# Optimization experiments

Measured on AMD Instinct MI355X. Metric: run time of the kernel, lower is better.

Reference implementation:

```python
import jax, jax.numpy as jnp
import numpy as np

E, B, L, H1, H2, C = 8, 4096, 512, 1024, 512, 40


def setup_inputs() -> dict:
    key = jax.random.key(0)
    ks = jax.random.split(key, 9)
    return {
        "x_s": jax.random.normal(ks[0], (B, L), jnp.float32),
        "x_p": jax.random.normal(ks[1], (B, L), jnp.float32),
        "W1": jax.random.normal(ks[2], (E, 2 * L, H1), jnp.float32) / np.sqrt(2 * L).astype(np.float32),
        "b1": jax.random.normal(ks[3], (E, H1), jnp.float32) * 0.01,
        "W2": jax.random.normal(ks[4], (E, H1, H2), jnp.float32) / np.sqrt(H1).astype(np.float32),
        "b2": jax.random.normal(ks[5], (E, H2), jnp.float32) * 0.01,
        "W3": jax.random.normal(ks[6], (E, H2, C), jnp.float32) / np.sqrt(H2).astype(np.float32),
        "b3": jax.random.normal(ks[7], (E, C), jnp.float32) * 0.01,
        "sub_module_label": jax.random.randint(ks[8], (B,), 0, E, dtype=jnp.int32),
        "sub_id": 0,
    }


def reference(x_s, x_p, W1, b1, W2, b2, W3, b3, sub_module_label, sub_id):
    # Encoders (EEGNet/SCN/DCN) abstracted as identity: x_s / x_p are latent features.
    # Cls_HEAD.forward: x = cat([x_p, x_s], dim=1); per-sample routed 3-layer ELU MLP head.
    # Dropout is identity in eval mode.
    x = jnp.concatenate([x_p, x_s], axis=1)                      # [B, 2L]
    h = jax.nn.elu(jnp.einsum('bi,eih->ebh', x, W1) + b1[:, None, :])   # [E, B, H1]
    h = jax.nn.elu(jnp.einsum('ebh,ehk->ebk', h, W2) + b2[:, None, :])  # [E, B, H2]
    out_all = jnp.einsum('ebk,ekc->ebc', h, W3) + b3[:, None, :]        # [E, B, C]
    # select each sample's routed expert output
    bidx = jnp.arange(x.shape[0])
    return out_all[sub_module_label, bidx]                       # [B, C]
```

## Files before the change

kernel.cpp:

```cpp
#include <hip/hip_runtime.h>
#include <hip/hip_bf16.h>
#include <math.h>

#define En   8
#define Bn   4096
#define Ln   512
#define K1n  1024
#define H1n  1024
#define H2n  512
#define Cn   40
#define NP3  48
#define NTR  72

typedef unsigned short u16;
typedef __attribute__((ext_vector_type(8))) short bf16x8;
typedef __attribute__((ext_vector_type(4))) float f32x4;

__device__ __forceinline__ u16 f2b(float f) {
    union { float f; unsigned int u; } v; v.f = f;
    unsigned int r = v.u + 0x7FFF + ((v.u >> 16) & 1);
    return (u16)(r >> 16);
}

__device__ __forceinline__ void g2l16(const void* g, void* l) {
    __builtin_amdgcn_global_load_lds(
        (const __attribute__((address_space(1))) unsigned int*)(unsigned long long)g,
        (__attribute__((address_space(3))) unsigned int*)(unsigned int)(unsigned long long)l,
        16, 0, 0);
}

__device__ __forceinline__ void wtrans64(
    const float* __restrict__ Wsrc, u16* __restrict__ Wdst,
    int K, int N, int k0, int n0, int tid, float* sm )
{
    #pragma unroll
    for (int s = 0; s < 4; s++) {
        int idx = tid + s * 256;
        int kk = idx >> 4, c4 = (idx & 15) * 4;
        float4 v = *(const float4*)&Wsrc[(size_t)(k0 + kk) * N + n0 + c4];
        float* row = sm + kk * 65 + c4;
        row[0] = v.x; row[1] = v.y; row[2] = v.z; row[3] = v.w;
    }
    __syncthreads();
    #pragma unroll
    for (int s = 0; s < 4; s++) {
        int idx = tid + s * 256;
        int nn = idx >> 4, kc = (idx & 15) * 4;
        ushort4 o = make_ushort4(f2b(sm[(kc + 0) * 65 + nn]), f2b(sm[(kc + 1) * 65 + nn]),
                                 f2b(sm[(kc + 2) * 65 + nn]), f2b(sm[(kc + 3) * 65 + nn]));
        *(ushort4*)&Wdst[(size_t)(n0 + nn) * K + k0 + kc] = o;
    }
}

#define P1_TOT (1 + 256 + 2048)

__global__ __launch_bounds__(256) void prep1_kernel(
    const float* __restrict__ xs, const float* __restrict__ xp,
    const float* __restrict__ W1, const int* __restrict__ label,
    int* __restrict__ meta, int* __restrict__ perm,
    u16* __restrict__ Xb, u16* __restrict__ W1t)
{
    __shared__ __align__(16) float sm[64 * 65];
    const int bid = blockIdx.x;
    const int tid = threadIdx.x;

    if (bid == 0) {
        int* cnt = (int*)sm;
        int* off = cnt + En;
        if (tid < En) cnt[tid] = 0;
        __syncthreads();
        for (int b = tid; b < Bn; b += 256) atomicAdd(&cnt[label[b]], 1);
        __syncthreads();
        if (tid == 0) {
            int run = 0;
            for (int e = 0; e < En; e++) { off[e] = run; run += cnt[e]; }
            off[En] = run;
        }
        __syncthreads();
        if (tid < En) cnt[tid] = off[tid];
        __syncthreads();
        for (int b = tid; b < Bn; b += 256) {
            int e = label[b];
            perm[atomicAdd(&cnt[e], 1)] = b;
        }
        if (tid <= En) meta[tid] = off[tid];
    } else if (bid < 257) {
        int r0 = (bid - 1) * 16;
        #pragma unroll 4
        for (int s = 0; s < 16; s++) {
            int r = r0 + s;
            int k = tid * 4;
            const float* src = (k < Ln) ? (xp + (size_t)r * Ln + k)
                                        : (xs + (size_t)r * Ln + (k - Ln));
            float4 v = *(const float4*)src;
            *(ushort4*)&Xb[(size_t)r * K1n + k] =
                make_ushort4(f2b(v.x), f2b(v.y), f2b(v.z), f2b(v.w));
        }
    } else {
        int b = bid - 257;
        int e = b >> 8, rem = b & 255;
        int k0 = (rem >> 4) * 64, n0 = (rem & 15) * 64;
        wtrans64(W1 + (size_t)e * K1n * H1n, W1t + (size_t)e * H1n * K1n,
                 K1n, H1n, k0, n0, tid, sm);
    }
}

template <int K, int N, bool GATHER, bool FUSE3, bool PREP2>
__global__ __launch_bounds__(256) void mfma_gemm(
    const u16* __restrict__ A, const u16* __restrict__ Wt,
    const float* __restrict__ bias, const int* __restrict__ meta,
    const int* __restrict__ perm, u16* __restrict__ outb,
    const u16* __restrict__ Wt3, float* __restrict__ outf,
    const float* __restrict__ W2f, const float* __restrict__ W3f,
    const float* __restrict__ b3v, const int* __restrict__ labelv,
    u16* __restrict__ W2t_o, u16* __restrict__ W3t_o)
{
    constexpr int TM = 64, BK = 64;
    constexpr int T = K / BK;
    constexpr int NTC = N / 64;
    __shared__ __align__(16) u16 SM[16384];

    const int tid = threadIdx.x;
    const int bx = blockIdx.x;

    if (PREP2 && bx >= NTR * NTC) {
        int jb = bx - NTR * NTC;
        if (jb < 1024) {
            int e = jb >> 7, rem = jb & 127;
            int k0 = (rem >> 3) * 64, n0 = (rem & 7) * 64;
            wtrans64(W2f + (size_t)e * H1n * H2n, W2t_o + (size_t)e * H2n * H1n,
                     H1n, H2n, k0, n0, tid, (float*)SM);
        } else if (jb < 1024 + 128) {
            int b = jb - 1024;
            int e = b >> 4, k0 = (b & 15) * 32;
            const float* src = W3f + (size_t)e * H2n * Cn;
            u16* dst = W3t_o + (size_t)e * NP3 * H2n;
            float* t = (float*)SM;
            #pragma unroll
            for (int s = 0; s < 5; s++) {
                int idx = tid + s * 256;
                int kk = idx / Cn, nn = idx - kk * Cn;
                if (kk < 32) t[kk * 41 + nn] = src[(size_t)(k0 + kk) * Cn + nn];
            }
            __syncthreads();
            #pragma unroll
            for (int s = 0; s < 6; s++) {
                int idx = tid + s * 256;
                int nn = idx >> 5, kk = idx & 31;
                float v = (nn < Cn) ? t[kk * 41 + nn] : 0.f;
                dst[(size_t)nn * H2n + k0 + kk] = f2b(v);
            }
        } else {
            int b = jb - (1024 + 128);
            int r0 = b * 64;
            #pragma unroll
            for (int s = 0; s < 10; s++) {
                int idx = tid + s * 256;
                int r = r0 + idx / Cn;
                int c = idx - (idx / Cn) * Cn;
                outf[(size_t)r * Cn + c] = b3v[labelv[r] * Cn + c];
            }
        }
        return;
    }

    const int rt = bx % NTR;
    const int col0 = (bx / NTR) * 64;

    int expert = -1, row0 = 0, rowmax = 0, acc_t = 0;
    int prev = meta[0];
    #pragma unroll
    for (int e = 0; e < En; e++) {
        int nxt = meta[e + 1];
        int c = nxt - prev;
        int t = (c + TM - 1) / TM;
        if (expert < 0 && rt < acc_t + t) {
            expert = e; row0 = prev + (rt - acc_t) * TM; rowmax = nxt - 1;
        }
        acc_t += t; prev = nxt;
    }
    if (expert < 0) return;

    const u16* Wexp = Wt + (size_t)expert * N * K;

    const int lane = tid & 63;
    const int wid = tid >> 6;
    const int wm = (wid & 1) * 32;
    const int wn = (wid >> 1) * 32;
    const int l15 = lane & 15;
    const int lq = lane >> 4;

    const u16* aptr[2]; const u16* bptr[2];
    int aoff[2], boff[2];
    #pragma unroll
    for (int s = 0; s < 2; s++) {
        int idx = tid + s * 256;
        int rl = idx >> 3, c = idx & 7;
        int kq = c ^ (rl & 7);
        int rg = row0 + rl; if (rg > rowmax) rg = rowmax;
        if (GATHER) rg = perm[rg];
        aptr[s] = A + (size_t)rg * K + kq * 8;
        bptr[s] = Wexp + (size_t)(col0 + rl) * K + kq * 8;
        aoff[s] = idx * 8;
        boff[s] = 4096 + idx * 8;
    }
    const int csw = l15 & 7;

    f32x4 acc[2][2];
    #pragma unroll
    for (int i = 0; i < 2; i++)
        #pragma unroll
        for (int j = 0; j < 2; j++) acc[i][j] = (f32x4){0.f, 0.f, 0.f, 0.f};

    #pragma unroll
    for (int s = 0; s < 2; s++) {
        g2l16(aptr[s], &SM[aoff[s]]);
        g2l16(bptr[s], &SM[boff[s]]);
    }

    for (int t = 0; t < T; t++) {
        __syncthreads();
        const u16* As = &SM[(t & 1) * 8192];
        const u16* Bs = As + 4096;
        if (t + 1 < T) {
            int base = ((t + 1) & 1) * 8192;
            int ko = (t + 1) * BK;
            #pragma unroll
            for (int s = 0; s < 2; s++) {
                g2l16(aptr[s] + ko, &SM[base + aoff[s]]);
                g2l16(bptr[s] + ko, &SM[base + boff[s]]);
            }
        }
        #pragma unroll
        for (int h = 0; h < 2; h++) {
            const int ksw = ((h * 4 + lq) ^ csw) << 3;
            bf16x8 af[2], bf[2];
            #pragma unroll
            for (int i = 0; i < 2; i++)
                af[i] = *(const bf16x8*)&As[(wm + i * 16 + l15) * BK + ksw];
            #pragma unroll
            for (int j = 0; j < 2; j++)
                bf[j] = *(const bf16x8*)&Bs[(wn + j * 16 + l15) * BK + ksw];
            #pragma unroll
            for (int i = 0; i < 2; i++)
                #pragma unroll
                for (int j = 0; j < 2; j++)
                    acc[i][j] = __builtin_amdgcn_mfma_f32_16x16x32_bf16(
                        af[i], bf[j], acc[i][j], 0, 0, 0);
        }
    }

    if (!FUSE3) {
        #pragma unroll
        for (int i = 0; i < 2; i++) {
            #pragma unroll
            for (int j = 0; j < 2; j++) {
                int col = col0 + wn + j * 16 + l15;
                float bv = bias[expert * N + col];
                #pragma unroll
                for (int r = 0; r < 4; r++) {
                    int grow = row0 + wm + i * 16 + lq * 4 + r;
                    if (grow <= rowmax) {
                        float v = acc[i][j][r] + bv;
                        v = (v > 0.f) ? v : (expf(v) - 1.f);
                        outb[(size_t)grow * N + col] = f2b(v);
                    }
                }
            }
        }
    } else {
        __syncthreads();
        u16* H = &SM[0];
        #pragma unroll
        for (int i = 0; i < 2; i++) {
            #pragma unroll
            for (int j = 0; j < 2; j++) {
                int col = wn + j * 16 + l15;
                float bv = bias[expert * N + col0 + col];
                #pragma unroll
                for (int r = 0; r < 4; r++) {
                    float v = acc[i][j][r] + bv;
                    v = (v > 0.f) ? v : (expf(v) - 1.f);
                    H[(wm + i * 16 + lq * 4 + r) * 72 + col] = f2b(v);
                }
            }
        }
        __syncthreads();
        const int rh = wid * 16;
        f32x4 a3[3];
        #pragma unroll
        for (int j = 0; j < 3; j++) a3[j] = (f32x4){0.f, 0.f, 0.f, 0.f};
        #pragma unroll
        for (int ki = 0; ki < 2; ki++) {
            bf16x8 ha = *(const bf16x8*)&H[(rh + l15) * 72 + ki * 32 + lq * 8];
            #pragma unroll
            for (int j = 0; j < 3; j++) {
                bf16x8 wb = *(const bf16x8*)
                    &Wt3[((size_t)expert * NP3 + j * 16 + l15) * H2n + col0 + ki * 32 + lq * 8];
                a3[j] = __builtin_amdgcn_mfma_f32_16x16x32_bf16(ha, wb, a3[j], 0, 0, 0);
            }
        }
        #pragma unroll
        for (int j = 0; j < 3; j++) {
            int col = j * 16 + l15;
            if (col < Cn) {
                #pragma unroll
                for (int r = 0; r < 4; r++) {
                    int grow = row0 + rh + lq * 4 + r;
                    if (grow <= rowmax)
                        atomicAdd(&outf[(size_t)perm[grow] * Cn + col], a3[j][r]);
                }
            }
        }
    }
}

extern "C" void kernel_launch(void* const* d_in, const int* in_sizes, int n_in,
                              void* d_out, int out_size, void* d_ws, size_t ws_size,
                              hipStream_t stream)
{
    const float* xs = (const float*)d_in[0];
    const float* xp = (const float*)d_in[1];
    const float* W1 = (const float*)d_in[2];
    const float* b1 = (const float*)d_in[3];
    const float* W2 = (const float*)d_in[4];
    const float* b2 = (const float*)d_in[5];
    const float* W3 = (const float*)d_in[6];
    const float* b3 = (const float*)d_in[7];
    const int* label = (const int*)d_in[8];
    float* out = (float*)d_out;

    char* ws = (char*)d_ws;
    int* meta = (int*)ws;
    int* perm = (int*)(ws + 64);
    u16* Xb  = (u16*)(ws + (64 << 10));
    u16* W1t = (u16*)(ws + (64 << 10) + (8  << 20));
    u16* W2t = (u16*)(ws + (64 << 10) + (24 << 20));
    u16* h1b = (u16*)(ws + (64 << 10) + (32 << 20));
    u16* W3t = (u16*)(ws + (64 << 10) + (40 << 20));

    prep1_kernel<<<P1_TOT, 256, 0, stream>>>(
        xs, xp, W1, label, meta, perm, Xb, W1t);

    mfma_gemm<K1n, H1n, true, false, true><<<72 * 16 + 1216, 256, 0, stream>>>(
        Xb, W1t, b1, meta, perm, h1b, nullptr, out,
        W2, W3, b3, label, W2t, W3t);

    mfma_gemm<H1n, H2n, false, true, false><<<72 * 8, 256, 0, stream>>>(
        h1b, W2t, b2, meta, perm, nullptr, W3t, out,
        nullptr, nullptr, nullptr, nullptr, nullptr, nullptr);
}
```

Baseline: 168.5 us.

## Template GEMM tile sizes and switch to larger tiles with BK=32

Makes the routed MFMA GEMM tile dimensions template parameters and uses 128x128 tiles for layer 1 and 128x64 for layer 2, with the K step halved to 32 and a matching new LDS swizzle. The fused layer-3 epilogue is generalized to cover multiple 16-row groups per wave. Larger tiles raise operand reuse per block and cut redundant global/LDS traffic. The cost is fewer blocks (320 per GEMM), more padding waste at expert boundaries, and twice as many barrier iterations along K.

New measurement: 173.1 us. 2.8% more time.

```diff
diff --git a/kernel.cpp b/kernel.cpp
--- a/kernel.cpp
+++ b/kernel.cpp
@@ -10,7 +10,6 @@
 #define H2n  512
 #define Cn   40
 #define NP3  48
-#define NTR  72
 
 typedef unsigned short u16;
 typedef __attribute__((ext_vector_type(8))) short bf16x8;
@@ -105,7 +104,7 @@
     }
 }
 
-template <int K, int N, bool GATHER, bool FUSE3, bool PREP2>
+template <int K, int N, int TM, int TN, bool GATHER, bool FUSE3, bool PREP2>
 __global__ __launch_bounds__(256) void mfma_gemm(
     const u16* __restrict__ A, const u16* __restrict__ Wt,
     const float* __restrict__ bias, const int* __restrict__ meta,
@@ -115,16 +114,23 @@
     const float* __restrict__ b3v, const int* __restrict__ labelv,
     u16* __restrict__ W2t_o, u16* __restrict__ W3t_o)
 {
-    constexpr int TM = 64, BK = 64;
-    constexpr int T = K / BK;
-    constexpr int NTC = N / 64;
-    __shared__ __align__(16) u16 SM[16384];
+    constexpr int BK    = 32;
+    constexpr int T     = K / BK;
+    constexpr int NTC   = N / TN;
+    constexpr int NTRk  = Bn / TM + En;
+    constexpr int ASLOT = TM * 4;
+    constexpr int BSLOT = TN * 4;
+    constexpr int STAGE = ASLOT + BSLOT;
+    constexpr int HSTR  = TN + 8;
+    constexpr int SMST  = 2 * STAGE * 8;
+    constexpr int SMU16 = (FUSE3 && (TM * HSTR) > SMST) ? (TM * HSTR) : SMST;
+    __shared__ __align__(16) u16 SM[SMU16];
 
     const int tid = threadIdx.x;
     const int bx = blockIdx.x;
 
-    if (PREP2 && bx >= NTR * NTC) {
-        int jb = bx - NTR * NTC;
+    if (PREP2 && bx >= NTRk * NTC) {
+        int jb = bx - NTRk * NTC;
         if (jb < 1024) {
             int e = jb >> 7, rem = jb & 127;
             int k0 = (rem >> 3) * 64, n0 = (rem & 7) * 64;
@@ -164,8 +170,8 @@
         return;
     }
 
-    const int rt = bx % NTR;
-    const int col0 = (bx / NTR) * 64;
+    const int rt = bx % NTRk;
+    const int col0 = (bx / NTRk) * TN;
 
     int expert = -1, row0 = 0, rowmax = 0, acc_t = 0;
     int prev = meta[0];
@@ -185,76 +191,81 @@
 
     const int lane = tid & 63;
     const int wid = tid >> 6;
-    const int wm = (wid & 1) * 32;
-    const int wn = (wid >> 1) * 32;
+    const int wm = (wid & 1) * (TM / 2);
+    const int wn = (wid >> 1) * (TN / 2);
     const int l15 = lane & 15;
     const int lq = lane >> 4;
 
-    const u16* aptr[2]; const u16* bptr[2];
-    int aoff[2], boff[2];
-    #pragma unroll
-    for (int s = 0; s < 2; s++) {
+    constexpr int ALOAD = ASLOT / 256;
+    constexpr int BLOAD = BSLOT / 256;
+    const u16* aptr[ALOAD]; int aoff[ALOAD];
+    const u16* bptr[BLOAD]; int boff[BLOAD];
+    #pragma unroll
+    for (int s = 0; s < ALOAD; s++) {
         int idx = tid + s * 256;
-        int rl = idx >> 3, c = idx & 7;
-        int kq = c ^ (rl & 7);
+        int rl = idx >> 2, c = idx & 3;
+        int kq = c ^ ((rl >> 1) & 3);
         int rg = row0 + rl; if (rg > rowmax) rg = rowmax;
         if (GATHER) rg = perm[rg];
         aptr[s] = A + (size_t)rg * K + kq * 8;
+        aoff[s] = idx * 8;
+    }
+    #pragma unroll
+    for (int s = 0; s < BLOAD; s++) {
+        int idx = tid + s * 256;
+        int rl = idx >> 2, c = idx & 3;
+        int kq = c ^ ((rl >> 1) & 3);
         bptr[s] = Wexp + (size_t)(col0 + rl) * K + kq * 8;
-        aoff[s] = idx * 8;
-        boff[s] = 4096 + idx * 8;
-    }
-    const int csw = l15 & 7;
-
-    f32x4 acc[2][2];
-    #pragma unroll
-    for (int i = 0; i < 2; i++)
-        #pragma unroll
-        for (int j = 0; j < 2; j++) acc[i][j] = (f32x4){0.f, 0.f, 0.f, 0.f};
-
-    #pragma unroll
-    for (int s = 0; s < 2; s++) {
-        g2l16(aptr[s], &SM[aoff[s]]);
-        g2l16(bptr[s], &SM[boff[s]]);
-    }
+        boff[s] = ASLOT * 8 + idx * 8;
+    }
+
+    constexpr int MI = TM / 32;
+    constexpr int NJ = TN / 32;
+    f32x4 acc[MI][NJ];
+    #pragma unroll
+    for (int i = 0; i < MI; i++)
+        #pragma unroll
+        for (int j = 0; j < NJ; j++) acc[i][j] = (f32x4){0.f, 0.f, 0.f, 0.f};
+
+    #pragma unroll
+    for (int s = 0; s < ALOAD; s++) g2l16(aptr[s], &SM[aoff[s]]);
+    #pragma unroll
+    for (int s = 0; s < BLOAD; s++) g2l16(bptr[s], &SM[boff[s]]);
+
+    const int cp = (lq ^ ((l15 >> 1) & 3)) * 8;
 
     for (int t = 0; t < T; t++) {
         __syncthreads();
-        const u16* As = &SM[(t & 1) * 8192];
-        const u16* Bs = As + 4096;
+        const u16* As = &SM[(t & 1) * (STAGE * 8)];
+        const u16* Bs = As + ASLOT * 8;
         if (t + 1 < T) {
-            int base = ((t + 1) & 1) * 8192;
+            int base = ((t + 1) & 1) * (STAGE * 8);
             int ko = (t + 1) * BK;
             #pragma unroll
-            for (int s = 0; s < 2; s++) {
-                g2l16(aptr[s] + ko, &SM[base + aoff[s]]);
-                g2l16(bptr[s] + ko, &SM[base + boff[s]]);
-            }
-        }
-        #pragma unroll
-        for (int h = 0; h < 2; h++) {
-            const int ksw = ((h * 4 + lq) ^ csw) << 3;
-            bf16x8 af[2], bf[2];
-            #pragma unroll
-            for (int i = 0; i < 2; i++)
-                af[i] = *(const bf16x8*)&As[(wm + i * 16 + l15) * BK + ksw];
-            #pragma unroll
-            for (int j = 0; j < 2; j++)
-                bf[j] = *(const bf16x8*)&Bs[(wn + j * 16 + l15) * BK + ksw];
-            #pragma unroll
-            for (int i = 0; i < 2; i++)
-                #pragma unroll
-                for (int j = 0; j < 2; j++)
-                    acc[i][j] = __builtin_amdgcn_mfma_f32_16x16x32_bf16(
-                        af[i], bf[j], acc[i][j], 0, 0, 0);
-        }
+            for (int s = 0; s < ALOAD; s++) g2l16(aptr[s] + ko, &SM[base + aoff[s]]);
+            #pragma unroll
+            for (int s = 0; s < BLOAD; s++) g2l16(bptr[s] + ko, &SM[base + boff[s]]);
+        }
+        bf16x8 af[MI], bf[NJ];
+        #pragma unroll
+        for (int i = 0; i < MI; i++)
+            af[i] = *(const bf16x8*)&As[(wm + i * 16 + l15) * BK + cp];
+        #pragma unroll
+        for (int j = 0; j < NJ; j++)
+            bf[j] = *(const bf16x8*)&Bs[(wn + j * 16 + l15) * BK + cp];
+        #pragma unroll
+        for (int i = 0; i < MI; i++)
+            #pragma unroll
+            for (int j = 0; j < NJ; j++)
+                acc[i][j] = __builtin_amdgcn_mfma_f32_16x16x32_bf16(
+                    af[i], bf[j], acc[i][j], 0, 0, 0);
     }
 
     if (!FUSE3) {
         #pragma unroll
-        for (int i = 0; i < 2; i++) {
-            #pragma unroll
-            for (int j = 0; j < 2; j++) {
+        for (int i = 0; i < MI; i++) {
+            #pragma unroll
+            for (int j = 0; j < NJ; j++) {
                 int col = col0 + wn + j * 16 + l15;
                 float bv = bias[expert * N + col];
                 #pragma unroll
@@ -272,32 +283,42 @@
         __syncthreads();
         u16* H = &SM[0];
         #pragma unroll
-        for (int i = 0; i < 2; i++) {
-            #pragma unroll
-            for (int j = 0; j < 2; j++) {
+        for (int i = 0; i < MI; i++) {
+            #pragma unroll
+            for (int j = 0; j < NJ; j++) {
                 int col = wn + j * 16 + l15;
                 float bv = bias[expert * N + col0 + col];
                 #pragma unroll
                 for (int r = 0; r < 4; r++) {
                     float v = acc[i][j][r] + bv;
                     v = (v > 0.f) ? v : (expf(v) - 1.f);
-                    H[(wm + i * 16 + lq * 4 + r) * 72 + col] = f2b(v);
+                    H[(wm + i * 16 + lq * 4 + r) * HSTR + col] = f2b(v);
                 }
             }
         }
         __syncthreads();
-        const int rh = wid * 16;
-        f32x4 a3[3];
-        #pragma unroll
-        for (int j = 0; j < 3; j++) a3[j] = (f32x4){0.f, 0.f, 0.f, 0.f};
-        #pragma unroll
-        for (int ki = 0; ki < 2; ki++) {
-            bf16x8 ha = *(const bf16x8*)&H[(rh + l15) * 72 + ki * 32 + lq * 8];
+        constexpr int RI = TM / 64;
+        constexpr int KC = TN / 32;
+        const int rh = wid * (TM / 4);
+        f32x4 a3[RI][3];
+        #pragma unroll
+        for (int ri = 0; ri < RI; ri++)
+            #pragma unroll
+            for (int j = 0; j < 3; j++) a3[ri][j] = (f32x4){0.f, 0.f, 0.f, 0.f};
+        #pragma unroll
+        for (int ki = 0; ki < KC; ki++) {
+            bf16x8 ha[RI];
+            #pragma unroll
+            for (int ri = 0; ri < RI; ri++)
+                ha[ri] = *(const bf16x8*)&H[(rh + ri * 16 + l15) * HSTR + ki * 32 + lq * 8];
             #pragma unroll
             for (int j = 0; j < 3; j++) {
                 bf16x8 wb = *(const bf16x8*)
                     &Wt3[((size_t)expert * NP3 + j * 16 + l15) * H2n + col0 + ki * 32 + lq * 8];
-                a3[j] = __builtin_amdgcn_mfma_f32_16x16x32_bf16(ha, wb, a3[j], 0, 0, 0);
+                #pragma unroll
+                for (int ri = 0; ri < RI; ri++)
+                    a3[ri][j] = __builtin_amdgcn_mfma_f32_16x16x32_bf16(
+                        ha[ri], wb, a3[ri][j], 0, 0, 0);
             }
         }
         #pragma unroll
@@ -305,10 +326,13 @@
             int col = j * 16 + l15;
             if (col < Cn) {
                 #pragma unroll
-                for (int r = 0; r < 4; r++) {
-                    int grow = row0 + rh + lq * 4 + r;
-                    if (grow <= rowmax)
-                        atomicAdd(&outf[(size_t)perm[grow] * Cn + col], a3[j][r]);
+                for (int ri = 0; ri < RI; ri++) {
+                    #pragma unroll
+                    for (int r = 0; r < 4; r++) {
+                        int grow = row0 + rh + ri * 16 + lq * 4 + r;
+                        if (grow <= rowmax)
+                            atomicAdd(&outf[(size_t)perm[grow] * Cn + col], a3[ri][j][r]);
+                    }
                 }
             }
         }
@@ -342,11 +366,11 @@
     prep1_kernel<<<P1_TOT, 256, 0, stream>>>(
         xs, xp, W1, label, meta, perm, Xb, W1t);
 
-    mfma_gemm<K1n, H1n, true, false, true><<<72 * 16 + 1216, 256, 0, stream>>>(
+    mfma_gemm<K1n, H1n, 128, 128, true, false, true><<<320 + 1216, 256, 0, stream>>>(
         Xb, W1t, b1, meta, perm, h1b, nullptr, out,
         W2, W3, b3, label, W2t, W3t);
 
-    mfma_gemm<H1n, H2n, false, true, false><<<72 * 8, 256, 0, stream>>>(
+    mfma_gemm<H1n, H2n, 128, 64, false, true, false><<<320, 256, 0, stream>>>(
         h1b, W2t, b2, meta, perm, nullptr, W3t, out,
         nullptr, nullptr, nullptr, nullptr, nullptr, nullptr);
 }
```
